# Kernel optimization log

Measured on AMD Instinct MI355X. Metric: run time of the kernel, lower is better.

## Reference

```python
import jax, jax.numpy as jnp
import numpy as np

B, S, V, E, H, OOV = 64, 512, 50257, 512, 1024, 12


def setup_inputs() -> dict:
    key = jax.random.key(0)
    ks = jax.random.split(key, 16)
    s = 0.02
    return {
        "input_idx": jax.random.randint(ks[0], (B,), 0, V),
        "encoded": jax.random.normal(ks[1], (B, S, 2 * H), dtype=jnp.float32),
        "encoded_idx": jax.random.randint(ks[2], (B, S), 0, V),
        "prev_state": jax.random.normal(ks[3], (B, H), dtype=jnp.float32),
        "weighted": jax.random.normal(ks[4], (B, 1, 2 * H), dtype=jnp.float32),
        "order": 1,
        "embed": jax.random.normal(ks[5], (V, E), dtype=jnp.float32) * s,
        "gru_wi": jax.random.normal(ks[6], (3 * H, E + 2 * H), dtype=jnp.float32) * s,
        "gru_wh": jax.random.normal(ks[7], (3 * H, H), dtype=jnp.float32) * s,
        "gru_bi": jnp.zeros((3 * H,), dtype=jnp.float32),
        "gru_bh": jnp.zeros((3 * H,), dtype=jnp.float32),
        "Ws_w": jax.random.normal(ks[8], (H, 2 * H), dtype=jnp.float32) * s,
        "Ws_b": jnp.zeros((H,), dtype=jnp.float32),
        "Wg_w": jax.random.normal(ks[9], (V, H), dtype=jnp.float32) * s,
        "Wg_b": jnp.zeros((V,), dtype=jnp.float32),
        "Wc_w": jax.random.normal(ks[10], (H, 2 * H), dtype=jnp.float32) * s,
        "Wc_b": jnp.zeros((H,), dtype=jnp.float32),
    }


def reference(input_idx, encoded, encoded_idx, prev_state, weighted, order,
              embed, gru_wi, gru_wh, gru_bi, gru_bh, Ws_w, Ws_b,
              Wg_w, Wg_b, Wc_w, Wc_b):
    if order == 0:  # static Python branch, matches the torch init branch
        prev_state = encoded[:, -1] @ Ws_w.T + Ws_b
        weighted = jnp.zeros((encoded.shape[0], 1, 2 * H), dtype=encoded.dtype)

    # one-step GRU (torch GRU gate order: r, z, n)
    x = jnp.concatenate([embed[input_idx], weighted[:, 0]], axis=-1)  # [B, E+2H]
    gi = x @ gru_wi.T + gru_bi
    gh = prev_state @ gru_wh.T + gru_bh
    gi_r, gi_z, gi_n = jnp.split(gi, 3, axis=-1)
    gh_r, gh_z, gh_n = jnp.split(gh, 3, axis=-1)
    r = jax.nn.sigmoid(gi_r + gh_r)
    z = jax.nn.sigmoid(gi_z + gh_z)
    n = jnp.tanh(gi_n + r * gh_n)
    state = (1.0 - z) * n + z * prev_state  # [B, H]

    # generate scores over vocab
    score_g = state @ Wg_w.T + Wg_b  # [B, V]

    # copy scores over source positions
    sc = jnp.tanh(jnp.einsum('bsd,hd->bsh', encoded, Wc_w) + Wc_b)  # [B, S, H]
    score_c = jnp.tanh(jnp.einsum('bsh,bh->bs', sc, state))
    score_c = score_c + jnp.where(encoded_idx == 0, -1000.0, 0.0)

    # joint softmax over generate + copy
    probs = jax.nn.softmax(jnp.concatenate([score_g, score_c], axis=1), axis=1)
    prob_g = probs[:, :V]
    prob_c = probs[:, V:]  # [B, S]

    # extend with OOV slots (+1e-4 as in torch code)
    prob_g = jnp.concatenate(
        [prob_g, jnp.full((prob_g.shape[0], OOV), 1e-4, dtype=prob_g.dtype)], axis=1)

    # prob_c -> vocab: scatter-add by source token id (== one-hot bmm in torch)
    def scatter_row(p, idx):
        return jnp.zeros((V + OOV,), dtype=p.dtype).at[idx].add(p)
    prob_c_to_g = jax.vmap(scatter_row)(prob_c, encoded_idx)  # [B, V+OOV]

    out = (prob_g + prob_c_to_g)[:, None, :]  # [B, 1, V+OOV]

    # attention restricted to source positions equal to input token, normalized
    m = (encoded_idx == input_idx[:, None]).astype(encoded.dtype)  # [B, S]
    ssum = m.sum(axis=1, keepdims=True)
    m = jnp.where(ssum > 1, m / jnp.maximum(ssum, 1.0), m)
    attn = prob_c * m
    weighted_out = jnp.einsum('bs,bsd->bd', attn, encoded)[:, None, :]  # [B, 1, 2H]

    return out, state, weighted_out
```

## Files before the change

kernel.cpp:

```cpp
#include <hip/hip_runtime.h>

#define B_    64
#define S_    512
#define V_    50257
#define E_    512
#define H_    1024
#define OOV_  12
#define VO_   (V_ + OOV_)
#define NTOT_ (V_ + S_)

typedef float  f32x4  __attribute__((ext_vector_type(4)));
typedef __bf16 bf16x8 __attribute__((ext_vector_type(8)));
typedef unsigned short ushort8 __attribute__((ext_vector_type(8)));

__device__ __forceinline__ unsigned short f2bf(float f) {
  union { float f; unsigned u; } c; c.f = f;
  unsigned r = c.u + 0x7FFFu + ((c.u >> 16) & 1u);
  return (unsigned short)(r >> 16);
}
__device__ __forceinline__ ushort8 cvt8(float4 u0, float4 u1) {
  ushort8 p;
  p[0] = f2bf(u0.x); p[1] = f2bf(u0.y); p[2] = f2bf(u0.z); p[3] = f2bf(u0.w);
  p[4] = f2bf(u1.x); p[5] = f2bf(u1.y); p[6] = f2bf(u1.z); p[7] = f2bf(u1.w);
  return p;
}

__global__ __launch_bounds__(256)
void cvt_bf16(const float* __restrict__ in, unsigned short* __restrict__ out, int n8)
{
  int i = blockIdx.x * 256 + threadIdx.x;
  const int stride = gridDim.x * 256;
  for (; i < n8; i += stride) {
    float4 u0 = ((const float4*)in)[2 * i];
    float4 u1 = ((const float4*)in)[2 * i + 1];
    ((ushort8*)out)[i] = cvt8(u0, u1);
  }
}

__global__ __launch_bounds__(256)
void build_x(const int* __restrict__ idx, const float* __restrict__ embed,
             const float* __restrict__ weighted, unsigned short* __restrict__ xb)
{
  const int t = blockIdx.x * 256 + threadIdx.x;
  if (t >= B_ * 320) return;
  const int m = t / 320, k = (t % 320) * 8;
  const float* src = (k < E_) ? &embed[(size_t)idx[m] * E_ + k]
                              : &weighted[(size_t)m * (2 * H_) + (k - E_)];
  float4 u0 = *(const float4*)src;
  float4 u1 = *(const float4*)(src + 4);
  ((ushort8*)xb)[t] = cvt8(u0, u1);
}

#define TILE 128
#define BK   64

template<int MODE, int ACVT, int BCVT, int XSWZ>
__global__ __launch_bounds__(256)
void gemm_bf(const unsigned short* __restrict__ Ab, const float* __restrict__ Af,
             const unsigned short* __restrict__ Bb, const float* __restrict__ Bf,
             const float* __restrict__ bias, const float* __restrict__ statev,
             float* __restrict__ out, int M, int N, int K, int ntn, int Kc)
{
  __shared__ unsigned short lds_a[TILE * BK];
  __shared__ unsigned short lds_b[TILE * BK];

  const int tid  = threadIdx.x;
  const int bid  = blockIdx.x;
  int m0, n0;
  if (XSWZ) {
    const int cpx = gridDim.x >> 6;
    const int xcd = bid & 7, s = bid >> 3;
    m0 = (xcd * cpx + (s >> 3)) * TILE;
    n0 = (s & 7) * TILE;
  } else {
    m0 = (bid / ntn) * TILE;
    n0 = (bid % ntn) * TILE;
  }

  const int lane = tid & 63;
  const int wave = tid >> 6;
  const int wrow = wave >> 1, wcol = wave & 1;
  const int lm   = lane & 15, quad = lane >> 4;

  f32x4 acc[4][4];
  #pragma unroll
  for (int i = 0; i < 4; ++i)
    #pragma unroll
    for (int j = 0; j < 4; ++j) { f32x4 z = {0.f, 0.f, 0.f, 0.f}; acc[i][j] = z; }

  const int k0   = blockIdx.y * Kc;
  const int kend = min(k0 + Kc, K);

  for (int kt = k0; kt < kend; kt += BK) {
    if (ACVT) {
      const int r = tid >> 1;
      const int grow = min(m0 + r, M - 1);
      const float* __restrict__ base = &Af[(size_t)grow * K + kt];
      #pragma unroll
      for (int q = 0; q < 4; ++q) {
        const int j = (tid & 1) * 4 + q;
        float4 u0 = *(const float4*)(base + j * 8);
        float4 u1 = *(const float4*)(base + j * 8 + 4);
        *(ushort8*)&lds_a[r * BK + (j ^ (r & 7)) * 8] = cvt8(u0, u1);
      }
    } else {
      #pragma unroll
      for (int t = 0; t < 4; ++t) {
        const int r  = (wave * 4 + t) * 8 + (lane >> 3);
        const int jg = (lane & 7) ^ (r & 7);
        const int grow = min(m0 + r, M - 1);
        const unsigned short* g = &Ab[(size_t)grow * K + kt + jg * 8];
        __builtin_amdgcn_global_load_lds(
            (const __attribute__((address_space(1))) void*)g,
            (__attribute__((address_space(3))) void*)&lds_a[(wave * 4 + t) * 512],
            16, 0, 0);
      }
    }
    if (BCVT) {
      const int r = tid >> 1;
      const int grow = min(n0 + r, N - 1);
      const float* __restrict__ base = &Bf[(size_t)grow * K + kt];
      #pragma unroll
      for (int q = 0; q < 4; ++q) {
        const int j = (tid & 1) * 4 + q;
        float4 u0 = *(const float4*)(base + j * 8);
        float4 u1 = *(const float4*)(base + j * 8 + 4);
        *(ushort8*)&lds_b[r * BK + (j ^ (r & 7)) * 8] = cvt8(u0, u1);
      }
    } else {
      #pragma unroll
      for (int t = 0; t < 4; ++t) {
        const int r  = (wave * 4 + t) * 8 + (lane >> 3);
        const int jg = (lane & 7) ^ (r & 7);
        const int grow = min(n0 + r, N - 1);
        const unsigned short* g = &Bb[(size_t)grow * K + kt + jg * 8];
        __builtin_amdgcn_global_load_lds(
            (const __attribute__((address_space(1))) void*)g,
            (__attribute__((address_space(3))) void*)&lds_b[(wave * 4 + t) * 512],
            16, 0, 0);
      }
    }
    __syncthreads();

    #pragma unroll
    for (int ks = 0; ks < BK; ks += 32) {
      const int c0 = ks >> 3;
      bf16x8 av[4], bv[4];
      #pragma unroll
      for (int i = 0; i < 4; ++i) {
        const int r = wrow * 64 + i * 16 + lm;
        av[i] = *(const bf16x8*)&lds_a[r * BK + (((c0 + quad) ^ (lm & 7)) * 8)];
      }
      #pragma unroll
      for (int j = 0; j < 4; ++j) {
        const int r = wcol * 64 + j * 16 + lm;
        bv[j] = *(const bf16x8*)&lds_b[r * BK + (((c0 + quad) ^ (lm & 7)) * 8)];
      }
      #pragma unroll
      for (int i = 0; i < 4; ++i)
        #pragma unroll
        for (int j = 0; j < 4; ++j)
          acc[i][j] = __builtin_amdgcn_mfma_f32_16x16x32_bf16(av[i], bv[j], acc[i][j], 0, 0, 0);
    }
    __syncthreads();
  }

  if (MODE == 0) {
    #pragma unroll
    for (int i = 0; i < 4; ++i) {
      const int rbase = m0 + wrow * 64 + i * 16 + quad * 4;
      #pragma unroll
      for (int j = 0; j < 4; ++j) {
        const int col = n0 + wcol * 64 + j * 16 + lm;
        if (col < N) {
          const float bv2 = bias[col];
          #pragma unroll
          for (int r = 0; r < 4; ++r) {
            const int row = rbase + r;
            if (row < M) out[(size_t)row * N + col] = acc[i][j][r] + bv2;
          }
        }
      }
    }
  } else if (MODE == 1) {
    float* rowsum = (float*)lds_b;
    if (tid < TILE) rowsum[tid] = 0.f;
    __syncthreads();
    #pragma unroll
    for (int i = 0; i < 4; ++i) {
      #pragma unroll
      for (int r = 0; r < 4; ++r) {
        const int rloc = wrow * 64 + i * 16 + quad * 4 + r;
        const int row  = m0 + rloc;
        const int b    = row >> 9;
        float p = 0.f;
        #pragma unroll
        for (int j = 0; j < 4; ++j) {
          const int col = wcol * 64 + j * 16 + lm;
          const float v = acc[i][j][r] + bias[col];
          p += tanhf(v) * statev[b * H_ + col];
        }
        p += __shfl_xor(p, 1);
        p += __shfl_xor(p, 2);
        p += __shfl_xor(p, 4);
        p += __shfl_xor(p, 8);
        if (lm == 0) atomicAdd(&rowsum[rloc], p);
      }
    }
    __syncthreads();
    if (tid < TILE) atomicAdd(&out[m0 + tid], rowsum[tid]);
  } else {
    #pragma unroll
    for (int i = 0; i < 4; ++i) {
      const int rbase = m0 + wrow * 64 + i * 16 + quad * 4;
      #pragma unroll
      for (int j = 0; j < 4; ++j) {
        const int col = n0 + wcol * 64 + j * 16 + lm;
        if (col < N) {
          #pragma unroll
          for (int r = 0; r < 4; ++r) {
            const int row = rbase + r;
            if (row < M) atomicAdd(&out[(size_t)row * N + col], acc[i][j][r]);
          }
        }
      }
    }
  }
}

__global__ __launch_bounds__(256)
void gru_combine(const float* __restrict__ gis, const float* __restrict__ ghs,
                 const float* __restrict__ prev, float* __restrict__ state,
                 unsigned short* __restrict__ st_bf,
                 const float* __restrict__ bi, const float* __restrict__ bh)
{
  const int idx = blockIdx.x * 256 + threadIdx.x;
  const int b = idx >> 10, h = idx & (H_ - 1);
  const float* gib = gis + (size_t)b * 3 * H_;
  const float* ghb = ghs + (size_t)b * 3 * H_;
  const float gr = gib[h]          + bi[h];
  const float hr = ghb[h]          + bh[h];
  const float gz = gib[H_ + h]     + bi[H_ + h];
  const float hz = ghb[H_ + h]     + bh[H_ + h];
  const float gn = gib[2 * H_ + h] + bi[2 * H_ + h];
  const float hn = ghb[2 * H_ + h] + bh[2 * H_ + h];
  const float r = 1.f / (1.f + expf(-(gr + hr)));
  const float z = 1.f / (1.f + expf(-(gz + hz)));
  const float n = tanhf(gn + r * hn);
  const float s = (1.f - z) * n + z * prev[idx];
  state[idx] = s;
  st_bf[idx] = f2bf(s);
}

#define CH  2048
#define NCH 25

__global__ __launch_bounds__(256)
void softmax_chunk(const float* __restrict__ score_g, const float* __restrict__ acc_c,
                   const int* __restrict__ eidx, float* __restrict__ mc, float* __restrict__ lc)
{
  const int b = blockIdx.y, c = blockIdx.x, tid = threadIdx.x;
  const int start = c * CH;
  const int end   = min(start + CH, NTOT_);
  __shared__ float red[4];

  float lmax = -1e30f;
  for (int i = start + tid; i < end; i += 256) {
    float v;
    if (i < V_) v = score_g[(size_t)b * V_ + i];
    else {
      const int s = i - V_;
      v = tanhf(acc_c[b * S_ + s]) + (eidx[b * S_ + s] == 0 ? -1000.f : 0.f);
    }
    lmax = fmaxf(lmax, v);
  }
  #pragma unroll
  for (int o = 32; o > 0; o >>= 1) lmax = fmaxf(lmax, __shfl_xor(lmax, o));
  if ((tid & 63) == 0) red[tid >> 6] = lmax;
  __syncthreads();
  lmax = fmaxf(fmaxf(red[0], red[1]), fmaxf(red[2], red[3]));
  __syncthreads();

  float lsum = 0.f;
  for (int i = start + tid; i < end; i += 256) {
    float v;
    if (i < V_) v = score_g[(size_t)b * V_ + i];
    else {
      const int s = i - V_;
      v = tanhf(acc_c[b * S_ + s]) + (eidx[b * S_ + s] == 0 ? -1000.f : 0.f);
    }
    lsum += expf(v - lmax);
  }
  #pragma unroll
  for (int o = 32; o > 0; o >>= 1) lsum += __shfl_xor(lsum, o);
  if ((tid & 63) == 0) red[tid >> 6] = lsum;
  __syncthreads();
  if (tid == 0) {
    mc[b * NCH + c] = lmax;
    lc[b * NCH + c] = red[0] + red[1] + red[2] + red[3];
  }
}

__global__ void softmax_combine(const float* __restrict__ mc, const float* __restrict__ lc,
                                float* __restrict__ Mrow, float* __restrict__ invL)
{
  const int b = threadIdx.x;
  float M = -1e30f;
  for (int c = 0; c < NCH; ++c) M = fmaxf(M, mc[b * NCH + c]);
  float L = 0.f;
  for (int c = 0; c < NCH; ++c) L += lc[b * NCH + c] * expf(mc[b * NCH + c] - M);
  Mrow[b] = M;
  invL[b] = 1.f / L;
}

__global__ __launch_bounds__(256)
void write_probg(const float* __restrict__ score_g, const float* __restrict__ Mrow,
                 const float* __restrict__ invL, float* __restrict__ out)
{
  const int b = blockIdx.y;
  const int v = blockIdx.x * 256 + threadIdx.x;
  if (v >= VO_) return;
  float val;
  if (v < V_) val = expf(score_g[(size_t)b * V_ + v] - Mrow[b]) * invL[b];
  else        val = 1e-4f;
  out[(size_t)b * VO_ + v] = val;
}

__global__ __launch_bounds__(256)
void scatter_weighted(const float* __restrict__ acc_c, const int* __restrict__ eidx,
                      const int* __restrict__ input_idx, const float* __restrict__ encoded,
                      const float* __restrict__ Mrow, const float* __restrict__ invL,
                      float* __restrict__ out, float* __restrict__ wout)
{
  __shared__ float pv[S_];
  __shared__ int   mlist[S_];
  __shared__ int   mcnt;
  const int b = blockIdx.x, tid = threadIdx.x;
  if (tid == 0) mcnt = 0;
  __syncthreads();

  const int   ii = input_idx[b];
  const float M  = Mrow[b], il = invL[b];
  for (int s = tid; s < S_; s += 256) {
    const int e = eidx[b * S_ + s];
    const float v = tanhf(acc_c[b * S_ + s]) + (e == 0 ? -1000.f : 0.f);
    const float p = expf(v - M) * il;
    pv[s] = p;
    atomicAdd(&out[(size_t)b * VO_ + e], p);
    if (e == ii) { const int pos = atomicAdd(&mcnt, 1); mlist[pos] = s; }
  }
  __syncthreads();

  const int cnt = mcnt;
  const float norm = cnt > 1 ? 1.f / (float)cnt : 1.f;
  for (int d = tid; d < 2 * H_; d += 256) {
    float a = 0.f;
    for (int t2 = 0; t2 < cnt; ++t2) {
      const int s = mlist[t2];
      a += pv[s] * encoded[((size_t)b * S_ + s) * (2 * H_) + d];
    }
    wout[(size_t)b * 2 * H_ + d] = a * norm;
  }
}

extern "C" void kernel_launch(void* const* d_in, const int* in_sizes, int n_in,
                              void* d_out, int out_size, void* d_ws, size_t ws_size,
                              hipStream_t stream)
{
  const int*   input_idx   = (const int*)  d_in[0];
  const float* encoded     = (const float*)d_in[1];
  const int*   encoded_idx = (const int*)  d_in[2];
  const float* prev_state  = (const float*)d_in[3];
  const float* weighted    = (const float*)d_in[4];
  const float* embed       = (const float*)d_in[6];
  const float* gru_wi      = (const float*)d_in[7];
  const float* gru_wh      = (const float*)d_in[8];
  const float* gru_bi      = (const float*)d_in[9];
  const float* gru_bh      = (const float*)d_in[10];
  const float* Wg_w        = (const float*)d_in[13];
  const float* Wg_b        = (const float*)d_in[14];
  const float* Wc_w        = (const float*)d_in[15];
  const float* Wc_b        = (const float*)d_in[16];

  float* out0  = (float*)d_out;
  float* state = out0 + (size_t)B_ * VO_;
  float* wout  = state + (size_t)B_ * H_;

  float* score_g = (float*)d_ws;
  float* gis     = score_g + (size_t)B_ * V_;
  float* ghs     = gis + (size_t)B_ * 3 * H_;
  float* acc_c   = ghs + (size_t)B_ * 3 * H_;
  float* mc      = acc_c + (size_t)B_ * S_;
  float* lc      = mc + B_ * NCH;
  float* Mrow    = lc + B_ * NCH;
  float* invL    = Mrow + B_;

  unsigned short* ub = (unsigned short*)(invL + B_);
  ub = (unsigned short*)(((uintptr_t)ub + 15) & ~(uintptr_t)15);
  unsigned short* x_bf  = ub;  ub += (size_t)B_ * (E_ + 2 * H_);
  unsigned short* ps_bf = ub;  ub += (size_t)B_ * H_;
  unsigned short* st_bf = ub;  ub += (size_t)B_ * H_;
  unsigned short* wc_bf = ub;
  unsigned short* wi_bf = wc_bf + (size_t)H_ * 2 * H_;
  unsigned short* wh_bf = wi_bf + (size_t)3 * H_ * (E_ + 2 * H_);
  unsigned short* end_small = wh_bf + (size_t)3 * H_ * H_;
  unsigned short* wg_bf  = end_small;
  unsigned short* end_wg = wg_bf + (size_t)V_ * H_;
  unsigned short* enc_bf = end_wg;
  unsigned short* end_enc = enc_bf + (size_t)B_ * S_ * 2 * H_;

  const bool cv_small = ws_size >= (size_t)((char*)end_small - (char*)d_ws);
  const bool cv_wg    = ws_size >= (size_t)((char*)end_wg    - (char*)d_ws);
  const bool cv_enc   = ws_size >= (size_t)((char*)end_enc   - (char*)d_ws);

  hipMemsetAsync(acc_c, 0, (size_t)B_ * S_ * sizeof(float), stream);
  hipMemsetAsync(gis, 0, (size_t)2 * B_ * 3 * H_ * sizeof(float), stream);

  dim3 blk(256);

  build_x<<<80, blk, 0, stream>>>(input_idx, embed, weighted, x_bf);
  cvt_bf16<<<32, blk, 0, stream>>>(prev_state, ps_bf, B_ * H_ / 8);
  if (cv_small) {
    cvt_bf16<<<1024, blk, 0, stream>>>(Wc_w, wc_bf, H_ * 2 * H_ / 8);
    cvt_bf16<<<3840, blk, 0, stream>>>(gru_wi, wi_bf, 3 * H_ * (E_ + 2 * H_) / 8);
    cvt_bf16<<<1536, blk, 0, stream>>>(gru_wh, wh_bf, 3 * H_ * H_ / 8);
  }
  if (cv_wg)  cvt_bf16<<<8192, blk, 0, stream>>>(Wg_w, wg_bf, V_ * H_ / 8);
  if (cv_enc) cvt_bf16<<<8192, blk, 0, stream>>>(encoded, enc_bf, B_ * S_ * 2 * H_ / 8);

  if (cv_small) {
    gemm_bf<2,0,0,0><<<dim3(24, 8), blk, 0, stream>>>(x_bf, nullptr, wi_bf, nullptr,
                                           nullptr, nullptr, gis, B_, 3 * H_, E_ + 2 * H_, 24, 320);
    gemm_bf<2,0,0,0><<<dim3(24, 8), blk, 0, stream>>>(ps_bf, nullptr, wh_bf, nullptr,
                                           nullptr, nullptr, ghs, B_, 3 * H_, H_, 24, 128);
  } else {
    gemm_bf<2,0,1,0><<<dim3(24, 8), blk, 0, stream>>>(x_bf, nullptr, nullptr, gru_wi,
                                           nullptr, nullptr, gis, B_, 3 * H_, E_ + 2 * H_, 24, 320);
    gemm_bf<2,0,1,0><<<dim3(24, 8), blk, 0, stream>>>(ps_bf, nullptr, nullptr, gru_wh,
                                           nullptr, nullptr, ghs, B_, 3 * H_, H_, 24, 128);
  }
  gru_combine<<<(B_ * H_) / 256, blk, 0, stream>>>(gis, ghs, prev_state, state, st_bf,
                                                   gru_bi, gru_bh);

  if (cv_wg)
    gemm_bf<0,0,0,0><<<393, blk, 0, stream>>>(st_bf, nullptr, wg_bf, nullptr,
                                            Wg_b, nullptr, score_g, B_, V_, H_, 393, H_);
  else
    gemm_bf<0,0,1,0><<<393, blk, 0, stream>>>(st_bf, nullptr, nullptr, Wg_w,
                                            Wg_b, nullptr, score_g, B_, V_, H_, 393, H_);

  if (cv_enc && cv_small)
    gemm_bf<1,0,0,1><<<2048, blk, 0, stream>>>(enc_bf, nullptr, wc_bf, nullptr,
                                             Wc_b, state, acc_c, B_ * S_, H_, 2 * H_, 8, 2 * H_);
  else if (cv_enc)
    gemm_bf<1,0,1,1><<<2048, blk, 0, stream>>>(enc_bf, nullptr, nullptr, Wc_w,
                                             Wc_b, state, acc_c, B_ * S_, H_, 2 * H_, 8, 2 * H_);
  else if (cv_small)
    gemm_bf<1,1,0,1><<<2048, blk, 0, stream>>>(nullptr, encoded, wc_bf, nullptr,
                                             Wc_b, state, acc_c, B_ * S_, H_, 2 * H_, 8, 2 * H_);
  else
    gemm_bf<1,1,1,1><<<2048, blk, 0, stream>>>(nullptr, encoded, nullptr, Wc_w,
                                             Wc_b, state, acc_c, B_ * S_, H_, 2 * H_, 8, 2 * H_);

  softmax_chunk<<<dim3(NCH, B_), blk, 0, stream>>>(score_g, acc_c, encoded_idx, mc, lc);
  softmax_combine<<<1, B_, 0, stream>>>(mc, lc, Mrow, invL);
  write_probg<<<dim3((VO_ + 255) / 256, B_), blk, 0, stream>>>(score_g, Mrow, invL, out0);
  scatter_weighted<<<B_, blk, 0, stream>>>(acc_c, encoded_idx, input_idx, encoded,
                                           Mrow, invL, out0, wout);
}
```

Measured before the change: 893.2 us.

## Add 256x256 double-buffered MFMA kernel for copy-score GEMM and fold softmax combine

Adds a dedicated 512-thread GEMM for the large encoded×Wc projection. It uses 256x256 tiles, direct global-to-LDS loads with XOR swizzling, double buffering interleaved with MFMA quadrants, and an XCD-aware block mapping. The tanh·state row reduction is fused in the epilogue through LDS atomics, so only one global atomic per row is issued. The separate softmax_combine launch is removed and its per-row max and sum reduction is recomputed in each write_probg and scatter_weighted block. This saves a launch at the cost of redundant per-block work.

```diff
diff --git a/kernel.cpp b/kernel.cpp
--- a/kernel.cpp
+++ b/kernel.cpp
@@ -228,6 +228,171 @@
   }
 }
 
+#define READ_A256(la, rbase)                                                   \
+  { _Pragma("unroll") for (int fi = 0; fi < 4; ++fi)                           \
+    _Pragma("unroll") for (int k = 0; k < 2; ++k) {                            \
+      const int r = (rbase) + fi * 16 + lm;                                    \
+      af[fi][k] = *(const bf16x8*)&(la)[r * 64 + (((k * 4 + quad) ^ (lm & 7)) * 8)]; } }
+
+#define READ_B256(lb, rbase, BB)                                               \
+  { _Pragma("unroll") for (int fj = 0; fj < 2; ++fj)                           \
+    _Pragma("unroll") for (int k = 0; k < 2; ++k) {                            \
+      const int r = (rbase) + fj * 16 + lm;                                    \
+      BB[fj][k] = *(const bf16x8*)&(lb)[r * 64 + (((k * 4 + quad) ^ (lm & 7)) * 8)]; } }
+
+#define MFMA_QUAD(rh, ch, BB)                                                  \
+  { __builtin_amdgcn_s_setprio(1);                                            \
+    _Pragma("unroll") for (int fi = 0; fi < 4; ++fi)                           \
+    _Pragma("unroll") for (int fj = 0; fj < 2; ++fj)                           \
+    _Pragma("unroll") for (int k = 0; k < 2; ++k)                              \
+      acc[rh][fi][ch][fj] = __builtin_amdgcn_mfma_f32_16x16x32_bf16(           \
+          af[fi][k], BB[fj][k], acc[rh][fi][ch][fj], 0, 0, 0);                 \
+    __builtin_amdgcn_s_setprio(0); }
+
+#define BAR256() { __builtin_amdgcn_s_barrier(); asm volatile("" ::: "memory"); }
+
+__global__ __launch_bounds__(512)
+void gemm256_accc(const unsigned short* __restrict__ A,
+                  const unsigned short* __restrict__ Bw,
+                  const float* __restrict__ bias,
+                  const float* __restrict__ statev,
+                  float* __restrict__ out)
+{
+  __shared__ unsigned short lds_a[2][256 * 64];
+  __shared__ unsigned short lds_b[2][256 * 64];
+  __shared__ float rowsum[256];
+
+  const int tid = threadIdx.x;
+  const int bid = blockIdx.x;
+  const int xcd = bid & 7, s = bid >> 3;
+  const int m0 = (xcd * 16 + (s >> 2)) * 256;
+  const int n0 = (s & 3) * 256;
+
+  const int lane = tid & 63;
+  const int wave = tid >> 6;
+  const int wr   = wave >> 2;
+  const int wc   = wave & 3;
+  const int lm   = lane & 15, quad = lane >> 4;
+
+  const int srow = tid >> 3;
+  const int jg   = (tid & 7) ^ (srow & 7);
+
+  if (tid < 256) rowsum[tid] = 0.f;
+
+  f32x4 acc[2][4][2][2];
+  #pragma unroll
+  for (int rh = 0; rh < 2; ++rh)
+    #pragma unroll
+    for (int fi = 0; fi < 4; ++fi)
+      #pragma unroll
+      for (int ch = 0; ch < 2; ++ch)
+        #pragma unroll
+        for (int fj = 0; fj < 2; ++fj) { f32x4 z = {0.f,0.f,0.f,0.f}; acc[rh][fi][ch][fj] = z; }
+
+  const unsigned short* A0 = A  + (size_t)m0 * 2048;
+  const unsigned short* B0 = Bw + (size_t)n0 * 2048;
+
+  auto stage_half = [&](const unsigned short* gbase, int grow0,
+                        unsigned short* lbase, int kabs) {
+    #pragma unroll
+    for (int i = 0; i < 2; ++i) {
+      const int r = i * 64 + srow;
+      const unsigned short* g = gbase + (size_t)(grow0 + r) * 2048 + kabs + jg * 8;
+      __builtin_amdgcn_global_load_lds(
+          (const __attribute__((address_space(1))) void*)g,
+          (__attribute__((address_space(3))) void*)(lbase + i * 4096 + wave * 512),
+          16, 0, 0);
+    }
+  };
+
+  bf16x8 af[4][2], bl[2][2], bh[2][2];
+
+  stage_half(A0, 0,   lds_a[0],        0);
+  stage_half(B0, 0,   lds_b[0],        0);
+  stage_half(A0, 128, lds_a[0] + 8192, 0);
+  stage_half(B0, 128, lds_b[0] + 8192, 0);
+
+  for (int t = 0; t < 31; ++t) {
+    const int cur = t & 1, nb = cur ^ 1;
+    const int kn  = (t + 1) * 64;
+    unsigned short* la_c = lds_a[cur];
+    unsigned short* lb_c = lds_b[cur];
+
+    stage_half(A0, 0, lds_a[nb], kn);
+    asm volatile("s_waitcnt vmcnt(6)" ::: "memory");
+    BAR256();
+    READ_A256(la_c, wr * 64);
+    READ_B256(lb_c, wc * 32, bl);
+    MFMA_QUAD(0, 0, bl);
+
+    stage_half(B0, 0, lds_b[nb], kn);
+    asm volatile("s_waitcnt vmcnt(4)" ::: "memory");
+    BAR256();
+    READ_B256(lb_c, 128 + wc * 32, bh);
+    MFMA_QUAD(0, 1, bh);
+
+    stage_half(A0, 128, lds_a[nb] + 8192, kn);
+    BAR256();
+    READ_A256(la_c, 128 + wr * 64);
+    MFMA_QUAD(1, 0, bl);
+
+    stage_half(B0, 128, lds_b[nb] + 8192, kn);
+    BAR256();
+    MFMA_QUAD(1, 1, bh);
+  }
+
+  {
+    unsigned short* la_c = lds_a[1];
+    unsigned short* lb_c = lds_b[1];
+
+    asm volatile("s_waitcnt vmcnt(4)" ::: "memory");
+    BAR256();
+    READ_A256(la_c, wr * 64);
+    READ_B256(lb_c, wc * 32, bl);
+    MFMA_QUAD(0, 0, bl);
+
+    asm volatile("s_waitcnt vmcnt(0)" ::: "memory");
+    BAR256();
+    READ_B256(lb_c, 128 + wc * 32, bh);
+    MFMA_QUAD(0, 1, bh);
+
+    BAR256();
+    READ_A256(la_c, 128 + wr * 64);
+    MFMA_QUAD(1, 0, bl);
+
+    BAR256();
+    MFMA_QUAD(1, 1, bh);
+  }
+
+  __syncthreads();
+  #pragma unroll
+  for (int rh = 0; rh < 2; ++rh)
+    #pragma unroll
+    for (int fi = 0; fi < 4; ++fi)
+      #pragma unroll
+      for (int r = 0; r < 4; ++r) {
+        const int rloc = rh * 128 + wr * 64 + fi * 16 + quad * 4 + r;
+        const int grow = m0 + rloc;
+        const int b    = grow >> 9;
+        float p = 0.f;
+        #pragma unroll
+        for (int ch = 0; ch < 2; ++ch)
+          #pragma unroll
+          for (int fj = 0; fj < 2; ++fj) {
+            const int col = n0 + ch * 128 + wc * 32 + fj * 16 + lm;
+            const float v = acc[rh][fi][ch][fj][r] + bias[col];
+            p += tanhf(v) * statev[b * H_ + col];
+          }
+        p += __shfl_xor(p, 1);
+        p += __shfl_xor(p, 2);
+        p += __shfl_xor(p, 4);
+        p += __shfl_xor(p, 8);
+        if (lm == 0) atomicAdd(&rowsum[rloc], p);
+      }
+  __syncthreads();
+  if (tid < 256) atomicAdd(&out[m0 + tid], rowsum[tid]);
+}
+
 __global__ __launch_bounds__(256)
 void gru_combine(const float* __restrict__ gis, const float* __restrict__ ghs,
                  const float* __restrict__ prev, float* __restrict__ state,
@@ -301,27 +466,24 @@
   }
 }
 
-__global__ void softmax_combine(const float* __restrict__ mc, const float* __restrict__ lc,
-                                float* __restrict__ Mrow, float* __restrict__ invL)
-{
-  const int b = threadIdx.x;
-  float M = -1e30f;
-  for (int c = 0; c < NCH; ++c) M = fmaxf(M, mc[b * NCH + c]);
-  float L = 0.f;
-  for (int c = 0; c < NCH; ++c) L += lc[b * NCH + c] * expf(mc[b * NCH + c] - M);
-  Mrow[b] = M;
-  invL[b] = 1.f / L;
-}
-
 __global__ __launch_bounds__(256)
-void write_probg(const float* __restrict__ score_g, const float* __restrict__ Mrow,
-                 const float* __restrict__ invL, float* __restrict__ out)
-{
-  const int b = blockIdx.y;
-  const int v = blockIdx.x * 256 + threadIdx.x;
+void write_probg(const float* __restrict__ score_g, const float* __restrict__ mc,
+                 const float* __restrict__ lc, float* __restrict__ out)
+{
+  __shared__ float sM, sIL;
+  const int b = blockIdx.y, tid = threadIdx.x;
+  if (tid == 0) {
+    float M = -1e30f;
+    for (int c = 0; c < NCH; ++c) M = fmaxf(M, mc[b * NCH + c]);
+    float L = 0.f;
+    for (int c = 0; c < NCH; ++c) L += lc[b * NCH + c] * expf(mc[b * NCH + c] - M);
+    sM = M; sIL = 1.f / L;
+  }
+  __syncthreads();
+  const int v = blockIdx.x * 256 + tid;
   if (v >= VO_) return;
   float val;
-  if (v < V_) val = expf(score_g[(size_t)b * V_ + v] - Mrow[b]) * invL[b];
+  if (v < V_) val = expf(score_g[(size_t)b * V_ + v] - sM) * sIL;
   else        val = 1e-4f;
   out[(size_t)b * VO_ + v] = val;
 }
@@ -329,18 +491,26 @@
 __global__ __launch_bounds__(256)
 void scatter_weighted(const float* __restrict__ acc_c, const int* __restrict__ eidx,
                       const int* __restrict__ input_idx, const float* __restrict__ encoded,
-                      const float* __restrict__ Mrow, const float* __restrict__ invL,
+                      const float* __restrict__ mc, const float* __restrict__ lc,
                       float* __restrict__ out, float* __restrict__ wout)
 {
   __shared__ float pv[S_];
   __shared__ int   mlist[S_];
   __shared__ int   mcnt;
+  __shared__ float sM, sIL;
   const int b = blockIdx.x, tid = threadIdx.x;
-  if (tid == 0) mcnt = 0;
+  if (tid == 0) {
+    mcnt = 0;
+    float M = -1e30f;
+    for (int c = 0; c < NCH; ++c) M = fmaxf(M, mc[b * NCH + c]);
+    float L = 0.f;
+    for (int c = 0; c < NCH; ++c) L += lc[b * NCH + c] * expf(mc[b * NCH + c] - M);
+    sM = M; sIL = 1.f / L;
+  }
   __syncthreads();
 
   const int   ii = input_idx[b];
-  const float M  = Mrow[b], il = invL[b];
+  const float M  = sM, il = sIL;
   for (int s = tid; s < S_; s += 256) {
     const int e = eidx[b * S_ + s];
     const float v = tanhf(acc_c[b * S_ + s]) + (e == 0 ? -1000.f : 0.f);
@@ -392,10 +562,8 @@
   float* acc_c   = ghs + (size_t)B_ * 3 * H_;
   float* mc      = acc_c + (size_t)B_ * S_;
   float* lc      = mc + B_ * NCH;
-  float* Mrow    = lc + B_ * NCH;
-  float* invL    = Mrow + B_;
-
-  unsigned short* ub = (unsigned short*)(invL + B_);
+
+  unsigned short* ub = (unsigned short*)(lc + B_ * NCH);
   ub = (unsigned short*)(((uintptr_t)ub + 15) & ~(uintptr_t)15);
   unsigned short* x_bf  = ub;  ub += (size_t)B_ * (E_ + 2 * H_);
   unsigned short* ps_bf = ub;  ub += (size_t)B_ * H_;
@@ -449,10 +617,9 @@
     gemm_bf<0,0,1,0><<<393, blk, 0, stream>>>(st_bf, nullptr, nullptr, Wg_w,
                                             Wg_b, nullptr, score_g, B_, V_, H_, 393, H_);
 
-  if (cv_enc && cv_small)
-    gemm_bf<1,0,0,1><<<2048, blk, 0, stream>>>(enc_bf, nullptr, wc_bf, nullptr,
-                                             Wc_b, state, acc_c, B_ * S_, H_, 2 * H_, 8, 2 * H_);
-  else if (cv_enc)
+  if (cv_enc && cv_small) {
+    gemm256_accc<<<512, 512, 0, stream>>>(enc_bf, wc_bf, Wc_b, state, acc_c);
+  } else if (cv_enc)
     gemm_bf<1,0,1,1><<<2048, blk, 0, stream>>>(enc_bf, nullptr, nullptr, Wc_w,
                                              Wc_b, state, acc_c, B_ * S_, H_, 2 * H_, 8, 2 * H_);
   else if (cv_small)
@@ -463,8 +630,7 @@
                                              Wc_b, state, acc_c, B_ * S_, H_, 2 * H_, 8, 2 * H_);
 
   softmax_chunk<<<dim3(NCH, B_), blk, 0, stream>>>(score_g, acc_c, encoded_idx, mc, lc);
-  softmax_combine<<<1, B_, 0, stream>>>(mc, lc, Mrow, invL);
-  write_probg<<<dim3((VO_ + 255) / 256, B_), blk, 0, stream>>>(score_g, Mrow, invL, out0);
+  write_probg<<<dim3((VO_ + 255) / 256, B_), blk, 0, stream>>>(score_g, mc, lc, out0);
   scatter_weighted<<<B_, blk, 0, stream>>>(acc_c, encoded_idx, input_idx, encoded,
-                                           Mrow, invL, out0, wout);
-}
+                                           mc, lc, out0, wout);
+}
```

Result: slower. 915.2 us (+2.5%).
